# Optimization experiments

Hardware: AMD Instinct MI355X
Metric: run time of the kernel (lower is better)

## Reference

```python
import jax, jax.numpy as jnp
import numpy as np

HID = 2048
NH = 16
NKV = 16
HD = HID // NH          # 128
ROPE_BASE = 100000.0
ROPE_SCALE = 4.0
B, L = 2, 2048
NEG = -1e9


def rope(x, offset=0):
    # x: [B, NH, L, HD]; half-split (rotate-half) RoPE with linear scaling
    Lx = x.shape[2]
    D = HD // 2
    pos = (jnp.arange(offset, offset + Lx, dtype=jnp.float32) / ROPE_SCALE)  # [L]
    freq = jnp.exp(-jnp.arange(D, dtype=jnp.float32) * (np.log(ROPE_BASE) / D))  # [D]
    m_theta = pos[:, None] * freq[None, :]          # [L, D]
    cos, sin = jnp.cos(m_theta), jnp.sin(m_theta)
    x1, x2 = x[..., :D], x[..., D:]
    rx1 = x1 * cos - x2 * sin
    rx2 = x1 * sin + x2 * cos
    return jnp.concatenate([rx1, rx2], axis=-1)


def setup_inputs() -> dict:
    key = jax.random.key(0)
    ks = jax.random.split(key, 5)
    x = jax.random.normal(ks[0], (B, L, HID), dtype=jnp.float32)
    # additive causal mask [1,1,L,L]
    mask = jnp.triu(jnp.full((L, L), NEG, dtype=jnp.float32), k=1)[None, None]
    Wq = jax.random.normal(ks[1], (HID, NH * HD), dtype=jnp.float32) * 0.02
    Wk = jax.random.normal(ks[2], (HID, NKV * HD), dtype=jnp.float32) * 0.02
    Wv = jax.random.normal(ks[3], (HID, NKV * HD), dtype=jnp.float32) * 0.02
    Wo = jax.random.normal(ks[4], (NH * HD, HID), dtype=jnp.float32) * 0.02
    return {"x": x, "mask": mask, "Wq": Wq, "Wk": Wk, "Wv": Wv, "Wo": Wo}


def reference(x, mask, Wq, Wk, Wv, Wo):
    b, l, _ = x.shape
    scale = HD ** -0.5
    q = (x @ Wq).reshape(b, l, NH, HD).transpose(0, 2, 1, 3)    # [B,NH,L,HD]
    k = (x @ Wk).reshape(b, l, NKV, HD).transpose(0, 2, 1, 3)
    v = (x @ Wv).reshape(b, l, NKV, HD).transpose(0, 2, 1, 3)
    rep = NH // NKV
    if rep > 1:
        k = jnp.repeat(k, rep, axis=1)
        v = jnp.repeat(v, rep, axis=1)
    q = rope(q)
    k = rope(k)
    scores = scale * jnp.einsum('bhqd,bhkd->bhqk', q, k)        # [B,NH,L,L]
    scores = scores + mask
    attn = jax.nn.softmax(scores, axis=-1)
    out = jnp.einsum('bhqk,bhkd->bhqd', attn, v)                # [B,NH,L,HD]
    out = out.transpose(0, 2, 1, 3).reshape(b, l, NH * HD)
    return out @ Wo
```

## Files before the change

### kernel.cpp

```cpp
#include <hip/hip_runtime.h>
#include <math.h>

#define BB   2
#define LL   2048
#define HIDD 2048
#define NHH  16
#define HDD  128
#define QKN  4096
#define THR2 11.5416f
#define EST  136

typedef unsigned short u16;
typedef float  f32x4 __attribute__((ext_vector_type(4)));
typedef __bf16 bf16x8 __attribute__((ext_vector_type(8)));

static __device__ __forceinline__ float exp2_fast(float x){
  return __builtin_amdgcn_exp2f(x);
}
static __device__ __forceinline__ u16 f2bf(float x){
  unsigned u = __float_as_uint(x);
  return (u16)((u + 0x7fffu + ((u >> 16) & 1u)) >> 16);
}
static __device__ __forceinline__ float bf2f(u16 b){
  return __uint_as_float(((unsigned)b) << 16);
}
static __device__ __forceinline__ void gl_lds16(const void* g, void* l){
  __builtin_amdgcn_global_load_lds(
      (__attribute__((address_space(1))) void*)(void*)g,
      (__attribute__((address_space(3))) void*)l,
      16, 0, 0);
}


__global__ void cvt_f32_bf16_k(const float* __restrict__ src, u16* __restrict__ dst, int n4){
  int i = blockIdx.x * blockDim.x + threadIdx.x;
  if (i >= n4) return;
  float4 v = ((const float4*)src)[i];
  ushort4 o;
  o.x = f2bf(v.x); o.y = f2bf(v.y); o.z = f2bf(v.z); o.w = f2bf(v.w);
  ((ushort4*)dst)[i] = o;
}

__global__ void rope_table_k(float2* __restrict__ tab){
  int idx = blockIdx.x * blockDim.x + threadIdx.x;
  int l = idx >> 6, d = idx & 63;
  float fr = __expf(-(float)d * 0.17988946f);
  float th = (float)l * 0.25f * fr;
  float s, c;
  sincosf(th, &s, &c);
  tab[idx] = make_float2(c, s);
}

__global__ __launch_bounds__(256) void transpose_cvt4_k(
    const float* __restrict__ Wq, const float* __restrict__ Wk,
    const float* __restrict__ Wv, const float* __restrict__ Wo,
    u16* __restrict__ Wt, u16* __restrict__ Wot)
{
  __shared__ u16 t[64][66];
  const int z = blockIdx.z;
  const float* src = (z == 0) ? Wq : (z == 1) ? Wk : (z == 2) ? Wv : Wo;
  u16* dst = (z == 3) ? Wot : (Wt + (size_t)z * 2048 * 2048);
  const int c0 = blockIdx.x * 64, r0 = blockIdx.y * 64;
  const int tid = threadIdx.x;

  #pragma unroll
  for (int i = 0; i < 4; i++){
    int r  = i * 16 + (tid >> 4);
    int c4 = (tid & 15) * 4;
    float4 v = *(const float4*)&src[(size_t)(r0 + r) * 2048 + c0 + c4];
    t[c4 + 0][r] = f2bf(v.x);
    t[c4 + 1][r] = f2bf(v.y);
    t[c4 + 2][r] = f2bf(v.z);
    t[c4 + 3][r] = f2bf(v.w);
  }
  __syncthreads();
  #pragma unroll
  for (int i = 0; i < 2; i++){
    int c  = i * 32 + (tid >> 3);
    int rs = (tid & 7) * 8;
    const unsigned* p = (const unsigned*)&t[c][rs];
    unsigned w0 = p[0], w1 = p[1], w2 = p[2], w3 = p[3];
    u16* d = &dst[(size_t)(c0 + c) * 2048 + r0 + rs];
    ((unsigned*)d)[0] = w0; ((unsigned*)d)[1] = w1;
    ((unsigned*)d)[2] = w2; ((unsigned*)d)[3] = w3;
  }
}


__global__ __launch_bounds__(256) void gemm_qkv_k(
    const u16* __restrict__ A, const u16* __restrict__ Bt,
    u16* __restrict__ qk, u16* __restrict__ vt,
    const float2* __restrict__ rtab, int M, int N, int K)
{
  __shared__ __align__(16) u16 SH[17408];
  u16* As = SH;
  u16* Bs = SH + 8192;
  const int tid = threadIdx.x, lane = tid & 63, wv = tid >> 6;
  const int wr = wv >> 1, wc = wv & 1;
  const int m0 = blockIdx.y * 128, n0 = blockIdx.x * 128;
  const int rq = lane >> 4, cl = lane & 15;

  const f32x4 Z = {0.f, 0.f, 0.f, 0.f};
  f32x4 acc[4][4];
  #pragma unroll
  for (int m = 0; m < 4; m++)
    #pragma unroll
    for (int n = 0; n < 4; n++) acc[m][n] = Z;

  for (int kt = 0; kt < K; kt += 64){
    #pragma unroll
    for (int i = 0; i < 4; i++){
      int fb = (i * 4 + wv) * 64;
      int p  = (fb + lane) * 16;
      int r  = p >> 7;
      int cbs = (p & 127) ^ ((r & 7) << 4);
      gl_lds16(A  + (size_t)(m0 + r) * K + kt + (cbs >> 1), &As[fb * 8]);
      gl_lds16(Bt + (size_t)(n0 + r) * K + kt + (cbs >> 1), &Bs[fb * 8]);
    }
    __syncthreads();
    #pragma unroll
    for (int ks = 0; ks < 2; ks++){
      const int kb = ks * 64 + rq * 16;
      bf16x8 a[4], b[4];
      #pragma unroll
      for (int m = 0; m < 4; m++){
        int r = wr * 64 + m * 16 + cl;
        a[m] = *(const bf16x8*)((const char*)As + r * 128 + (kb ^ ((r & 7) << 4)));
      }
      #pragma unroll
      for (int n = 0; n < 4; n++){
        int r = wc * 64 + n * 16 + cl;
        b[n] = *(const bf16x8*)((const char*)Bs + r * 128 + (kb ^ ((r & 7) << 4)));
      }
      #pragma unroll
      for (int m = 0; m < 4; m++)
        #pragma unroll
        for (int n = 0; n < 4; n++)
          acc[m][n] = __builtin_amdgcn_mfma_f32_16x16x32_bf16(a[m], b[n], acc[m][n], 0, 0, 0);
    }
    __syncthreads();
  }

  const int hd  = n0 >> 7;
  const int sec = hd >> 4;
  const int hh  = hd & 15;

  #pragma unroll
  for (int m = 0; m < 4; m++){
    int gr0 = wr * 64 + m * 16 + rq * 4;
    #pragma unroll
    for (int n = 0; n < 4; n++){
      int gc = wc * 64 + n * 16 + cl;
      #pragma unroll
      for (int rr = 0; rr < 4; rr++)
        SH[(gr0 + rr) * EST + gc] = f2bf(acc[m][n][rr]);
    }
  }
  __syncthreads();

  if (sec < 2){
    const float fsc = (sec == 0) ? 0.12753375f : 1.0f;
    const int r = tid >> 1, dbase = (tid & 1) * 32;
    const int l = (m0 + r) & (LL - 1);
    const float2* tab = rtab + l * 64 + dbase;
    const u16* srow = &SH[r * EST];
    u16* orow = qk + (size_t)(m0 + r) * QKN + hd * 128;
    #pragma unroll
    for (int g = 0; g < 4; g++){
      bf16x8 x1v = *(const bf16x8*)(srow + dbase + g * 8);
      bf16x8 x2v = *(const bf16x8*)(srow + dbase + 64 + g * 8);
      bf16x8 o1, o2;
      #pragma unroll
      for (int i = 0; i < 8; i++){
        float2 cs = tab[g * 8 + i];
        float x1 = (float)x1v[i], x2 = (float)x2v[i];
        o1[i] = (__bf16)((x1 * cs.x - x2 * cs.y) * fsc);
        o2[i] = (__bf16)((x1 * cs.y + x2 * cs.x) * fsc);
      }
      *(bf16x8*)(orow + dbase + g * 8)      = o1;
      *(bf16x8*)(orow + dbase + 64 + g * 8) = o2;
    }
  } else {
    const int d = tid >> 1, l0 = (tid & 1) * 64;
    const int bh = ((m0 >> 11) << 4) + hh;
    u16* vrow = vt + ((size_t)bh * HDD + d) * LL + (m0 & (LL - 1)) + l0;
    #pragma unroll
    for (int g = 0; g < 8; g++){
      bf16x8 o;
      #pragma unroll
      for (int i = 0; i < 8; i++)
        o[i] = *(__bf16*)&SH[(l0 + g * 8 + i) * EST + d];
      *(bf16x8*)(vrow + g * 8) = o;
    }
  }
}


#define G2_STAGE(kt, bsel) do {                                                           \
  _Pragma("unroll")                                                                       \
  for (int i_ = 0; i_ < 2; i_++){                            \
    int c_ = ((i_ * 8 + wv) * 64) + lane;                                                 \
    int p_ = c_ * 16;                                                                     \
    int r_ = p_ >> 7; int cb_ = (p_ & 127) ^ ((r_ & 7) << 4);                             \
    gl_lds16(A + (size_t)(m0 + r_) * K + (kt) + (cb_ >> 1),                               \
             &AB[bsel][((i_ * 8 + wv) * 64) * 8]);                                        \
  }                                                                                       \
  _Pragma("unroll")                                                                       \
  for (int i_ = 0; i_ < 4; i_++){                            \
    int c_ = ((i_ * 8 + wv) * 64) + lane;                                                 \
    int p_ = c_ * 16;                                                                     \
    int r_ = p_ >> 7; int cb_ = (p_ & 127) ^ ((r_ & 7) << 4);                             \
    gl_lds16(Bt + (size_t)(n0 + r_) * K + (kt) + (cb_ >> 1),                              \
             &AB[bsel][8192 + ((i_ * 8 + wv) * 64) * 8]);                                 \
  }                                                                                       \
} while(0)

template<int OUT_BF16>
__global__ __launch_bounds__(512, 1) void gemm_bt2_k(
    const u16* __restrict__ A, const u16* __restrict__ Bt,
    void* __restrict__ Cout, int M, int N, int K)
{
  __shared__ __align__(16) u16 AB[2][24576];
  const int tid = threadIdx.x, lane = tid & 63, wv = tid >> 6;
  const int wr = wv >> 2, wc = wv & 3;
  const int m0 = blockIdx.y * 128, n0 = blockIdx.x * 256;
  const int rq = lane >> 4, cl = lane & 15;
  const int NT = K >> 6;

  const f32x4 Z = {0.f, 0.f, 0.f, 0.f};
  f32x4 acc[4][4];
  #pragma unroll
  for (int m = 0; m < 4; m++)
    #pragma unroll
    for (int n = 0; n < 4; n++) acc[m][n] = Z;

  G2_STAGE(0, 0);
  G2_STAGE(64, 1);
  asm volatile("s_waitcnt vmcnt(6)");
  __builtin_amdgcn_sched_barrier(0);
  __builtin_amdgcn_s_barrier();

  int cur = 0;
  for (int t = 0; t < NT; t++){
    const char* As_ = (const char*)&AB[cur][0];
    const char* Bs_ = (const char*)&AB[cur][8192];

    #pragma unroll
    for (int ks = 0; ks < 2; ks++){
      const int kb = ks * 64 + rq * 16;
      bf16x8 a[4], b[4];
      #pragma unroll
      for (int m = 0; m < 4; m++){
        int r = wr * 64 + m * 16 + cl;
        a[m] = *(const bf16x8*)(As_ + r * 128 + (kb ^ ((r & 7) << 4)));
      }
      #pragma unroll
      for (int n = 0; n < 4; n++){
        int r = wc * 64 + n * 16 + cl;
        b[n] = *(const bf16x8*)(Bs_ + r * 128 + (kb ^ ((r & 7) << 4)));
      }
      __builtin_amdgcn_s_setprio(1);
      #pragma unroll
      for (int m = 0; m < 4; m++)
        #pragma unroll
        for (int n = 0; n < 4; n++)
          acc[m][n] = __builtin_amdgcn_mfma_f32_16x16x32_bf16(a[m], b[n], acc[m][n], 0, 0, 0);
      __builtin_amdgcn_s_setprio(0);
    }

    __builtin_amdgcn_sched_barrier(0);
    __builtin_amdgcn_s_barrier();

    if (t + 2 < NT){
      G2_STAGE((t + 2) * 64, cur);
      asm volatile("s_waitcnt vmcnt(6)");
    } else {
      asm volatile("s_waitcnt vmcnt(0)");
    }
    __builtin_amdgcn_sched_barrier(0);
    __builtin_amdgcn_s_barrier();
    cur ^= 1;
  }

  #pragma unroll
  for (int m = 0; m < 4; m++){
    int gr0 = m0 + wr * 64 + m * 16 + rq * 4;
    #pragma unroll
    for (int n = 0; n < 4; n++){
      int gc = n0 + wc * 64 + n * 16 + cl;
      #pragma unroll
      for (int rr = 0; rr < 4; rr++){
        if (OUT_BF16) ((u16*)Cout)[(size_t)(gr0 + rr) * N + gc] = f2bf(acc[m][n][rr]);
        else          ((float*)Cout)[(size_t)(gr0 + rr) * N + gc] = acc[m][n][rr];
      }
    }
  }
}


#define STAGE_K(jj, bsel) do {                                                            \
  _Pragma("unroll")                                                                       \
  for (int i_ = 0; i_ < 4; i_++){                                                         \
    int fb_ = (i_ * 4 + wv) * 64;                                                         \
    int p_  = (fb_ + lane) * 16;                                                          \
    int r_ = p_ >> 8; int cb_ = (p_ & 255) ^ ((r_ & 7) << 4);                             \
    gl_lds16(qk + (size_t)(b * LL + (jj) * 64 + r_) * QKN + 2048 + h * HDD + (cb_ >> 1),  \
             &Kb[bsel][fb_ * 8]);                                                         \
  }                                                                                       \
} while(0)

#define STAGE_V(jj, bsel) do {                                                            \
  _Pragma("unroll")                                                                       \
  for (int i_ = 0; i_ < 4; i_++){                                                         \
    int fb_ = (i_ * 4 + wv) * 64;                                                         \
    int p_  = (fb_ + lane) * 16;                                                          \
    int r_ = p_ >> 7; int cb_ = (p_ & 127) ^ ((r_ & 7) << 4);                             \
    gl_lds16(vt + (size_t)(bh * HDD + r_) * LL + (jj) * 64 + (cb_ >> 1),                  \
             &Vb[bsel][fb_ * 8]);                                                         \
  }                                                                                       \
} while(0)

__global__ __launch_bounds__(256, 2) void attn_k(
    const u16* __restrict__ qk, const u16* __restrict__ vt,
    u16* __restrict__ aout)
{
  __shared__ __align__(16) u16 Kb[2][64 * 128];
  __shared__ __align__(16) u16 Vb[2][128 * 64];
  __shared__ __align__(16) u16 Ps[4][1024];
  const int tid = threadIdx.x, lane = tid & 63, wv = tid >> 6;
  const int bh = blockIdx.x;
  const int pr = blockIdx.y;
  const int b = bh >> 4, h = bh & 15;
  const int rq = lane >> 4, cl = lane & 15;

  bf16x8 ones;
  #pragma unroll
  for (int i = 0; i < 8; i++) ones[i] = (__bf16)1.0f;
  const f32x4 Z = {0.f, 0.f, 0.f, 0.f};

  int cur = 0;
  STAGE_V(0, 0);
  STAGE_K(0, 0);

  #pragma unroll
  for (int ph = 0; ph < 2; ph++){
    const int qt = ph ? pr : (31 - pr);
    const int nj = qt + 1;

    bf16x8 qf[4];
    {
      const u16* qb = qk + (size_t)(b * LL + qt * 64 + wv * 16 + cl) * QKN + h * HDD + rq * 8;
      #pragma unroll
      for (int ks = 0; ks < 4; ks++) qf[ks] = *(const bf16x8*)(qb + ks * 32);
    }

    f32x4 acco[8], accl;
    float mst[4];
    #pragma unroll
    for (int n = 0; n < 8; n++) acco[n] = Z;
    accl = Z;
    #pragma unroll
    for (int rr = 0; rr < 4; rr++) mst[rr] = -INFINITY;

    for (int j = 0; j < nj; j++){
      const bool sn = (j + 1 < nj) || (ph == 0);
      if (j + 1 < nj){      STAGE_V(j + 1, cur ^ 1); STAGE_K(j + 1, cur ^ 1); }
      else if (ph == 0){    STAGE_V(0,     cur ^ 1); STAGE_K(0,     cur ^ 1); }
      __builtin_amdgcn_sched_barrier(0);
      if (sn) asm volatile("s_waitcnt vmcnt(8)" ::: "memory");
      else    asm volatile("s_waitcnt vmcnt(0)" ::: "memory");
      __builtin_amdgcn_sched_barrier(0);
      __builtin_amdgcn_s_barrier();
      __builtin_amdgcn_sched_barrier(0);

      f32x4 sv[4];
      {
        const char* KsC = (const char*)&Kb[cur][0];
        #pragma unroll
        for (int ct = 0; ct < 4; ct++) sv[ct] = Z;
        #pragma unroll
        for (int ks = 0; ks < 4; ks++){
          const int kb = ks * 64 + rq * 16;
          #pragma unroll
          for (int ct = 0; ct < 4; ct++){
            int r = ct * 16 + cl;
            bf16x8 bfr = *(const bf16x8*)(KsC + r * 256 + (kb ^ ((r & 7) << 4)));
            sv[ct] = __builtin_amdgcn_mfma_f32_16x16x32_bf16(qf[ks], bfr, sv[ct], 0, 0, 0);
          }
        }
      }

      {
        char* pbase = (char*)&Ps[wv][0];
        const bool msk = (j == qt);

        float p4[4][4], lmx[4];
        #pragma unroll
        for (int rr = 0; rr < 4; rr++) lmx[rr] = -1e30f;
        const int qg = qt * 64 + wv * 16 + rq * 4;
        #pragma unroll
        for (int ct = 0; ct < 4; ct++){
          int col = j * 64 + ct * 16 + cl;
          #pragma unroll
          for (int rr = 0; rr < 4; rr++){
            float v = sv[ct][rr];
            if (msk && col > qg + rr) v = -1e30f;
            p4[ct][rr] = v;
            lmx[rr] = fmaxf(lmx[rr], v);
          }
        }
        float need = -1e30f;
        #pragma unroll
        for (int rr = 0; rr < 4; rr++) need = fmaxf(need, lmx[rr] - mst[rr]);
        if (__any(need > THR2)){
          float mx[4];
          #pragma unroll
          for (int rr = 0; rr < 4; rr++) mx[rr] = lmx[rr];
          #pragma unroll
          for (int off = 1; off < 16; off <<= 1)
            #pragma unroll
            for (int rr = 0; rr < 4; rr++)
              mx[rr] = fmaxf(mx[rr], __shfl_xor(mx[rr], off, 64));
          #pragma unroll
          for (int rr = 0; rr < 4; rr++){
            float mn  = fmaxf(mst[rr], mx[rr]);
            float fsc = exp2_fast(mst[rr] - mn);
            mst[rr] = mn;
            accl[rr] *= fsc;
            #pragma unroll
            for (int n = 0; n < 8; n++) acco[n][rr] *= fsc;
          }
        }
        #pragma unroll
        for (int ct = 0; ct < 4; ct++)
          #pragma unroll
          for (int rr = 0; rr < 4; rr++){
            float e = exp2_fast(p4[ct][rr] - mst[rr]);
            int wr = rq * 4 + rr;
            *(u16*)(pbase + wr * 128 + (((ct * 16 + cl) * 2) ^ ((wr & 7) << 4))) = f2bf(e);
          }
      }

      {
        const char* VsC = (const char*)&Vb[cur][0];
        char* pbase = (char*)&Ps[wv][0];
        #pragma unroll
        for (int ks = 0; ks < 2; ks++){
          const int kvb = ks * 64 + rq * 16;
          bf16x8 pa = *(const bf16x8*)(pbase + cl * 128 + (kvb ^ ((cl & 7) << 4)));
          accl = __builtin_amdgcn_mfma_f32_16x16x32_bf16(pa, ones, accl, 0, 0, 0);
          #pragma unroll
          for (int n = 0; n < 8; n++){
            int r = n * 16 + cl;
            bf16x8 bfr = *(const bf16x8*)(VsC + r * 128 + (kvb ^ ((r & 7) << 4)));
            acco[n] = __builtin_amdgcn_mfma_f32_16x16x32_bf16(pa, bfr, acco[n], 0, 0, 0);
          }
        }
      }

      __builtin_amdgcn_sched_barrier(0);
      __builtin_amdgcn_s_barrier();
      __builtin_amdgcn_sched_barrier(0);
      cur ^= 1;
    }

    #pragma unroll
    for (int rr = 0; rr < 4; rr++){
      float inv = 1.0f / accl[rr];
      size_t grow = (size_t)(b * LL + qt * 64 + wv * 16 + rq * 4 + rr);
      #pragma unroll
      for (int n = 0; n < 8; n++)
        aout[grow * HIDD + h * HDD + n * 16 + cl] = f2bf(acco[n][rr] * inv);
    }
  }
}


extern "C" void kernel_launch(void* const* d_in, const int* in_sizes, int n_in,
                              void* d_out, int out_size, void* d_ws, size_t ws_size,
                              hipStream_t stream)
{
  const float* x  = (const float*)d_in[0];
  const float* Wq = (const float*)d_in[2];
  const float* Wk = (const float*)d_in[3];
  const float* Wv = (const float*)d_in[4];
  const float* Wo = (const float*)d_in[5];
  float* out = (float*)d_out;

  if (ws_size < 120586240ull) return;

  char* ws = (char*)d_ws;
  u16*    xb   = (u16*)(ws);
  u16*    Wt   = (u16*)(ws + 16777216ull);
  u16*    Wot  = (u16*)(ws + 41943040ull);
  u16*    qk   = (u16*)(ws + 50331648ull);
  u16*    vt   = (u16*)(ws + 83886080ull);
  u16*    aout = (u16*)(ws + 100663296ull);
  float2* rtab = (float2*)(ws + 117440512ull);

  cvt_f32_bf16_k<<<2097152 / 256, 256, 0, stream>>>(x, xb, 2097152);
  rope_table_k<<<131072 / 256, 256, 0, stream>>>(rtab);
  transpose_cvt4_k<<<dim3(32, 32, 4), 256, 0, stream>>>(Wq, Wk, Wv, Wo, Wt, Wot);

  gemm_qkv_k<<<dim3(6144 / 128, 4096 / 128), 256, 0, stream>>>(xb, Wt, qk, vt, rtab, 4096, 6144, 2048);

  attn_k<<<dim3(32, 16), 256, 0, stream>>>(qk, vt, aout);

  gemm_bt2_k<0><<<dim3(2048 / 256, 4096 / 128), 512, 0, stream>>>(aout, Wot, out, 4096, 2048, 2048);
}
```

Before: 259.5 us.

## Rewrite QKV GEMM with 256x256 tiles and ping-pong LDS prefetch pipeline

```diff
diff --git a/kernel.cpp b/kernel.cpp
--- a/kernel.cpp
+++ b/kernel.cpp
@@ -8,7 +8,7 @@
 #define HDD  128
 #define QKN  4096
 #define THR2 11.5416f
-#define EST  136
+#define EST2 264
 
 typedef unsigned short u16;
 typedef float  f32x4 __attribute__((ext_vector_type(4)));
@@ -87,110 +87,229 @@
 }
 
 
-__global__ __launch_bounds__(256) void gemm_qkv_k(
+#define STG_HALF(base_u16, src, rowbase, kt_) do {                                        \
+  _Pragma("unroll")                                                                       \
+  for (int i_ = 0; i_ < 2; i_++){                                                         \
+    int cb0_ = i_ * 512 + wv * 64;                           \
+    int c_   = cb0_ + lane;                                                               \
+    int r_   = c_ >> 3;                                       \
+    int cb_  = ((c_ & 7) << 4) ^ ((r_ & 7) << 4);                                         \
+    gl_lds16((src) + (size_t)((rowbase) + r_) * K + (kt_) + (cb_ >> 1),                   \
+             &SH[(base_u16) + cb0_ * 8]);                                                 \
+  }                                                                                       \
+} while(0)
+
+__global__ __launch_bounds__(512, 1) void gemm_qkv256_k(
     const u16* __restrict__ A, const u16* __restrict__ Bt,
     u16* __restrict__ qk, u16* __restrict__ vt,
-    const float2* __restrict__ rtab, int M, int N, int K)
+    const float2* __restrict__ rtab, int K)
 {
-  __shared__ __align__(16) u16 SH[17408];
-  u16* As = SH;
-  u16* Bs = SH + 8192;
+  __shared__ __align__(16) u16 SH[65536];
   const int tid = threadIdx.x, lane = tid & 63, wv = tid >> 6;
-  const int wr = wv >> 1, wc = wv & 1;
-  const int m0 = blockIdx.y * 128, n0 = blockIdx.x * 128;
+  const int wsr = wv >> 2, wsc = wv & 3;
+  const int m0 = blockIdx.y * 256, n0 = blockIdx.x * 256;
   const int rq = lane >> 4, cl = lane & 15;
+  const int NT = K >> 6;
 
   const f32x4 Z = {0.f, 0.f, 0.f, 0.f};
-  f32x4 acc[4][4];
-  #pragma unroll
-  for (int m = 0; m < 4; m++)
-    #pragma unroll
-    for (int n = 0; n < 4; n++) acc[m][n] = Z;
-
-  for (int kt = 0; kt < K; kt += 64){
-    #pragma unroll
-    for (int i = 0; i < 4; i++){
-      int fb = (i * 4 + wv) * 64;
-      int p  = (fb + lane) * 16;
-      int r  = p >> 7;
-      int cbs = (p & 127) ^ ((r & 7) << 4);
-      gl_lds16(A  + (size_t)(m0 + r) * K + kt + (cbs >> 1), &As[fb * 8]);
-      gl_lds16(Bt + (size_t)(n0 + r) * K + kt + (cbs >> 1), &Bs[fb * 8]);
-    }
+  f32x4 acc[2][2][4][2];
+  #pragma unroll
+  for (int i = 0; i < 2; i++)
+    #pragma unroll
+    for (int j = 0; j < 2; j++)
+      #pragma unroll
+      for (int mf = 0; mf < 4; mf++)
+        #pragma unroll
+        for (int nf = 0; nf < 2; nf++) acc[i][j][mf][nf] = Z;
+
+  STG_HALF(0,                 A,  m0 + 0,   0);
+  STG_HALF(32768,             Bt, n0 + 0,   0);
+  STG_HALF(8192,              A,  m0 + 128, 0);
+  STG_HALF(32768 + 8192,      Bt, n0 + 128, 0);
+  STG_HALF(16384,             A,  m0 + 0,   64);
+  STG_HALF(32768 + 16384,     Bt, n0 + 0,   64);
+
+  for (int t = 0; t < NT; t++){
+    const int X = t & 1;
+    const char* Ab = (const char*)SH + X * 32768;
+    const char* Bb = (const char*)SH + 65536 + X * 32768;
+    bf16x8 af[4][2], bfb[2][2];
+
+    __builtin_amdgcn_sched_barrier(0);
+    if (t == NT - 1) asm volatile("s_waitcnt vmcnt(0)" ::: "memory");
+    else             asm volatile("s_waitcnt vmcnt(4)" ::: "memory");
+    __builtin_amdgcn_sched_barrier(0);
+    __builtin_amdgcn_s_barrier();
+    __builtin_amdgcn_sched_barrier(0);
+    #pragma unroll
+    for (int mf = 0; mf < 4; mf++){
+      int gr = wsr * 64 + mf * 16 + cl;
+      #pragma unroll
+      for (int ks = 0; ks < 2; ks++)
+        af[mf][ks] = *(const bf16x8*)(Ab + gr * 128 + ((ks * 64 + rq * 16) ^ ((gr & 7) << 4)));
+    }
+    #pragma unroll
+    for (int nf = 0; nf < 2; nf++){
+      int gc = wsc * 32 + nf * 16 + cl;
+      #pragma unroll
+      for (int ks = 0; ks < 2; ks++)
+        bfb[nf][ks] = *(const bf16x8*)(Bb + gc * 128 + ((ks * 64 + rq * 16) ^ ((gc & 7) << 4)));
+    }
+    if (t + 1 < NT) STG_HALF(((t + 1) & 1) * 16384 + 8192, A, m0 + 128, (t + 1) * 64);
+    __builtin_amdgcn_sched_barrier(0);
+    asm volatile("s_waitcnt lgkmcnt(0)" ::: "memory");
+    __builtin_amdgcn_sched_barrier(0);
+    __builtin_amdgcn_s_setprio(1);
+    #pragma unroll
+    for (int mf = 0; mf < 4; mf++)
+      #pragma unroll
+      for (int nf = 0; nf < 2; nf++)
+        #pragma unroll
+        for (int ks = 0; ks < 2; ks++)
+          acc[0][0][mf][nf] = __builtin_amdgcn_mfma_f32_16x16x32_bf16(af[mf][ks], bfb[nf][ks], acc[0][0][mf][nf], 0, 0, 0);
+    __builtin_amdgcn_s_setprio(0);
+    __builtin_amdgcn_sched_barrier(0);
+
+    __builtin_amdgcn_s_barrier();
+    __builtin_amdgcn_sched_barrier(0);
+    #pragma unroll
+    for (int nf = 0; nf < 2; nf++){
+      int gc = 128 + wsc * 32 + nf * 16 + cl;
+      #pragma unroll
+      for (int ks = 0; ks < 2; ks++)
+        bfb[nf][ks] = *(const bf16x8*)(Bb + gc * 128 + ((ks * 64 + rq * 16) ^ ((gc & 7) << 4)));
+    }
+    if (t + 1 < NT) STG_HALF(32768 + ((t + 1) & 1) * 16384 + 8192, Bt, n0 + 128, (t + 1) * 64);
+    __builtin_amdgcn_sched_barrier(0);
+    asm volatile("s_waitcnt lgkmcnt(0)" ::: "memory");
+    __builtin_amdgcn_sched_barrier(0);
+    __builtin_amdgcn_s_setprio(1);
+    #pragma unroll
+    for (int mf = 0; mf < 4; mf++)
+      #pragma unroll
+      for (int nf = 0; nf < 2; nf++)
+        #pragma unroll
+        for (int ks = 0; ks < 2; ks++)
+          acc[0][1][mf][nf] = __builtin_amdgcn_mfma_f32_16x16x32_bf16(af[mf][ks], bfb[nf][ks], acc[0][1][mf][nf], 0, 0, 0);
+    __builtin_amdgcn_s_setprio(0);
+    __builtin_amdgcn_sched_barrier(0);
+
+    __builtin_amdgcn_s_barrier();
+    __builtin_amdgcn_sched_barrier(0);
+    #pragma unroll
+    for (int mf = 0; mf < 4; mf++){
+      int gr = 128 + wsr * 64 + mf * 16 + cl;
+      #pragma unroll
+      for (int ks = 0; ks < 2; ks++)
+        af[mf][ks] = *(const bf16x8*)(Ab + gr * 128 + ((ks * 64 + rq * 16) ^ ((gr & 7) << 4)));
+    }
+    #pragma unroll
+    for (int nf = 0; nf < 2; nf++){
+      int gc = wsc * 32 + nf * 16 + cl;
+      #pragma unroll
+      for (int ks = 0; ks < 2; ks++)
+        bfb[nf][ks] = *(const bf16x8*)(Bb + gc * 128 + ((ks * 64 + rq * 16) ^ ((gc & 7) << 4)));
+    }
+    if (t + 2 < NT) STG_HALF((t & 1) * 16384, A, m0 + 0, (t + 2) * 64);
+    __builtin_amdgcn_sched_barrier(0);
+    asm volatile("s_waitcnt lgkmcnt(0)" ::: "memory");
+    __builtin_amdgcn_sched_barrier(0);
+    __builtin_amdgcn_s_setprio(1);
+    #pragma unroll
+    for (int mf = 0; mf < 4; mf++)
+      #pragma unroll
+      for (int nf = 0; nf < 2; nf++)
+        #pragma unroll
+        for (int ks = 0; ks < 2; ks++)
+          acc[1][0][mf][nf] = __builtin_amdgcn_mfma_f32_16x16x32_bf16(af[mf][ks], bfb[nf][ks], acc[1][0][mf][nf], 0, 0, 0);
+    __builtin_amdgcn_s_setprio(0);
+    __builtin_amdgcn_sched_barrier(0);
+
+    __builtin_amdgcn_s_barrier();
+    __builtin_amdgcn_sched_barrier(0);
+    #pragma unroll
+    for (int nf = 0; nf < 2; nf++){
+      int gc = 128 + wsc * 32 + nf * 16 + cl;
+      #pragma unroll
+      for (int ks = 0; ks < 2; ks++)
+        bfb[nf][ks] = *(const bf16x8*)(Bb + gc * 128 + ((ks * 64 + rq * 16) ^ ((gc & 7) << 4)));
+    }
+    if (t + 2 < NT) STG_HALF(32768 + (t & 1) * 16384, Bt, n0 + 0, (t + 2) * 64);
+    __builtin_amdgcn_sched_barrier(0);
+    asm volatile("s_waitcnt lgkmcnt(0)" ::: "memory");
+    __builtin_amdgcn_sched_barrier(0);
+    __builtin_amdgcn_s_setprio(1);
+    #pragma unroll
+    for (int mf = 0; mf < 4; mf++)
+      #pragma unroll
+      for (int nf = 0; nf < 2; nf++)
+        #pragma unroll
+        for (int ks = 0; ks < 2; ks++)
+          acc[1][1][mf][nf] = __builtin_amdgcn_mfma_f32_16x16x32_bf16(af[mf][ks], bfb[nf][ks], acc[1][1][mf][nf], 0, 0, 0);
+    __builtin_amdgcn_s_setprio(0);
+    __builtin_amdgcn_sched_barrier(0);
+  }
+
+  const int sec = n0 >> 11;
+  const int hd2 = n0 >> 7;
+  u16* ES = SH;
+
+  #pragma unroll
+  for (int ih = 0; ih < 2; ih++){
     __syncthreads();
     #pragma unroll
-    for (int ks = 0; ks < 2; ks++){
-      const int kb = ks * 64 + rq * 16;
-      bf16x8 a[4], b[4];
-      #pragma unroll
-      for (int m = 0; m < 4; m++){
-        int r = wr * 64 + m * 16 + cl;
-        a[m] = *(const bf16x8*)((const char*)As + r * 128 + (kb ^ ((r & 7) << 4)));
-      }
-      #pragma unroll
-      for (int n = 0; n < 4; n++){
-        int r = wc * 64 + n * 16 + cl;
-        b[n] = *(const bf16x8*)((const char*)Bs + r * 128 + (kb ^ ((r & 7) << 4)));
-      }
-      #pragma unroll
-      for (int m = 0; m < 4; m++)
-        #pragma unroll
-        for (int n = 0; n < 4; n++)
-          acc[m][n] = __builtin_amdgcn_mfma_f32_16x16x32_bf16(a[m], b[n], acc[m][n], 0, 0, 0);
-    }
+    for (int j = 0; j < 2; j++)
+      #pragma unroll
+      for (int mf = 0; mf < 4; mf++){
+        int er = wsr * 64 + mf * 16 + rq * 4;
+        #pragma unroll
+        for (int nf = 0; nf < 2; nf++){
+          int ec = j * 128 + wsc * 32 + nf * 16 + cl;
+          #pragma unroll
+          for (int rr = 0; rr < 4; rr++)
+            ES[(er + rr) * EST2 + ec] = f2bf(acc[ih][j][mf][nf][rr]);
+        }
+      }
     __syncthreads();
-  }
-
-  const int hd  = n0 >> 7;
-  const int sec = hd >> 4;
-  const int hh  = hd & 15;
-
-  #pragma unroll
-  for (int m = 0; m < 4; m++){
-    int gr0 = wr * 64 + m * 16 + rq * 4;
-    #pragma unroll
-    for (int n = 0; n < 4; n++){
-      int gc = wc * 64 + n * 16 + cl;
-      #pragma unroll
-      for (int rr = 0; rr < 4; rr++)
-        SH[(gr0 + rr) * EST + gc] = f2bf(acc[m][n][rr]);
-    }
-  }
-  __syncthreads();
-
-  if (sec < 2){
-    const float fsc = (sec == 0) ? 0.12753375f : 1.0f;
-    const int r = tid >> 1, dbase = (tid & 1) * 32;
-    const int l = (m0 + r) & (LL - 1);
-    const float2* tab = rtab + l * 64 + dbase;
-    const u16* srow = &SH[r * EST];
-    u16* orow = qk + (size_t)(m0 + r) * QKN + hd * 128;
-    #pragma unroll
-    for (int g = 0; g < 4; g++){
-      bf16x8 x1v = *(const bf16x8*)(srow + dbase + g * 8);
-      bf16x8 x2v = *(const bf16x8*)(srow + dbase + 64 + g * 8);
-      bf16x8 o1, o2;
-      #pragma unroll
-      for (int i = 0; i < 8; i++){
-        float2 cs = tab[g * 8 + i];
-        float x1 = (float)x1v[i], x2 = (float)x2v[i];
-        o1[i] = (__bf16)((x1 * cs.x - x2 * cs.y) * fsc);
-        o2[i] = (__bf16)((x1 * cs.y + x2 * cs.x) * fsc);
-      }
-      *(bf16x8*)(orow + dbase + g * 8)      = o1;
-      *(bf16x8*)(orow + dbase + 64 + g * 8) = o2;
-    }
-  } else {
-    const int d = tid >> 1, l0 = (tid & 1) * 64;
-    const int bh = ((m0 >> 11) << 4) + hh;
-    u16* vrow = vt + ((size_t)bh * HDD + d) * LL + (m0 & (LL - 1)) + l0;
-    #pragma unroll
-    for (int g = 0; g < 8; g++){
-      bf16x8 o;
-      #pragma unroll
-      for (int i = 0; i < 8; i++)
-        o[i] = *(__bf16*)&SH[(l0 + g * 8 + i) * EST + d];
-      *(bf16x8*)(vrow + g * 8) = o;
+
+    if (sec < 2){
+      const float fsc = (sec == 0) ? 0.12753375f : 1.0f;
+      const int r = tid >> 2, cq = tid & 3;
+      const int j = cq >> 1, dbase = (cq & 1) * 32;
+      const int grow = m0 + ih * 128 + r;
+      const int l = grow & (LL - 1);
+      const float2* tab = rtab + l * 64 + dbase;
+      const u16* srow = &ES[r * EST2 + j * 128];
+      u16* orow = qk + (size_t)grow * QKN + n0 + j * 128;
+      #pragma unroll
+      for (int g = 0; g < 4; g++){
+        bf16x8 x1v = *(const bf16x8*)(srow + dbase + g * 8);
+        bf16x8 x2v = *(const bf16x8*)(srow + dbase + 64 + g * 8);
+        bf16x8 o1, o2;
+        #pragma unroll
+        for (int i8 = 0; i8 < 8; i8++){
+          float2 cs = tab[g * 8 + i8];
+          float x1 = (float)x1v[i8], x2 = (float)x2v[i8];
+          o1[i8] = (__bf16)((x1 * cs.x - x2 * cs.y) * fsc);
+          o2[i8] = (__bf16)((x1 * cs.y + x2 * cs.x) * fsc);
+        }
+        *(bf16x8*)(orow + dbase + g * 8)      = o1;
+        *(bf16x8*)(orow + dbase + 64 + g * 8) = o2;
+      }
+    } else {
+      const int c = tid >> 1, lh = tid & 1;
+      const int j = c >> 7, d = c & 127;
+      const int grow0 = m0 + ih * 128;
+      const int bh = ((grow0 >> 11) << 4) + (hd2 - 32 + j);
+      u16* vrow = vt + ((size_t)bh * HDD + d) * LL + (grow0 & (LL - 1)) + lh * 64;
+      #pragma unroll
+      for (int g = 0; g < 8; g++){
+        bf16x8 o;
+        #pragma unroll
+        for (int i8 = 0; i8 < 8; i8++)
+          o[i8] = *(__bf16*)&ES[(lh * 64 + g * 8 + i8) * EST2 + c];
+        *(bf16x8*)(vrow + g * 8) = o;
+      }
     }
   }
 }
@@ -502,7 +621,7 @@
   rope_table_k<<<131072 / 256, 256, 0, stream>>>(rtab);
   transpose_cvt4_k<<<dim3(32, 32, 4), 256, 0, stream>>>(Wq, Wk, Wv, Wo, Wt, Wot);
 
-  gemm_qkv_k<<<dim3(6144 / 128, 4096 / 128), 256, 0, stream>>>(xb, Wt, qk, vt, rtab, 4096, 6144, 2048);
+  gemm_qkv256_k<<<dim3(6144 / 256, 4096 / 256), 512, 0, stream>>>(xb, Wt, qk, vt, rtab, 2048);
 
   attn_k<<<dim3(32, 16), 256, 0, stream>>>(qk, vt, aout);
 
```

Measured after the change: 256.3 us (median of 3 runs). No clear change (-1.2%).

## Permute B rows so RoPE pairs land in registers, skip LDS staging for Q/K

Applied to the files above, without the earlier changes.

```diff
diff --git a/kernel.cpp b/kernel.cpp
--- a/kernel.cpp
+++ b/kernel.cpp
@@ -114,8 +114,9 @@
       int p  = (fb + lane) * 16;
       int r  = p >> 7;
       int cbs = (p & 127) ^ ((r & 7) << 4);
+      int sg = ((r >> 6) << 5) + (((r >> 4) & 1) << 4) + (((r >> 5) & 1) << 6) + (r & 15);
       gl_lds16(A  + (size_t)(m0 + r) * K + kt + (cbs >> 1), &As[fb * 8]);
-      gl_lds16(Bt + (size_t)(n0 + r) * K + kt + (cbs >> 1), &Bs[fb * 8]);
+      gl_lds16(Bt + (size_t)(n0 + sg) * K + kt + (cbs >> 1), &Bs[fb * 8]);
     }
     __syncthreads();
     #pragma unroll
@@ -145,42 +146,39 @@
   const int sec = hd >> 4;
   const int hh  = hd & 15;
 
-  #pragma unroll
-  for (int m = 0; m < 4; m++){
-    int gr0 = wr * 64 + m * 16 + rq * 4;
-    #pragma unroll
-    for (int n = 0; n < 4; n++){
-      int gc = wc * 64 + n * 16 + cl;
-      #pragma unroll
-      for (int rr = 0; rr < 4; rr++)
-        SH[(gr0 + rr) * EST + gc] = f2bf(acc[m][n][rr]);
-    }
-  }
-  __syncthreads();
-
   if (sec < 2){
     const float fsc = (sec == 0) ? 0.12753375f : 1.0f;
-    const int r = tid >> 1, dbase = (tid & 1) * 32;
-    const int l = (m0 + r) & (LL - 1);
-    const float2* tab = rtab + l * 64 + dbase;
-    const u16* srow = &SH[r * EST];
-    u16* orow = qk + (size_t)(m0 + r) * QKN + hd * 128;
-    #pragma unroll
-    for (int g = 0; g < 4; g++){
-      bf16x8 x1v = *(const bf16x8*)(srow + dbase + g * 8);
-      bf16x8 x2v = *(const bf16x8*)(srow + dbase + 64 + g * 8);
-      bf16x8 o1, o2;
-      #pragma unroll
-      for (int i = 0; i < 8; i++){
-        float2 cs = tab[g * 8 + i];
-        float x1 = (float)x1v[i], x2 = (float)x2v[i];
-        o1[i] = (__bf16)((x1 * cs.x - x2 * cs.y) * fsc);
-        o2[i] = (__bf16)((x1 * cs.y + x2 * cs.x) * fsc);
-      }
-      *(bf16x8*)(orow + dbase + g * 8)      = o1;
-      *(bf16x8*)(orow + dbase + 64 + g * 8) = o2;
+    const int d0 = wc * 32 + cl;
+    #pragma unroll
+    for (int m = 0; m < 4; m++){
+      #pragma unroll
+      for (int rr = 0; rr < 4; rr++){
+        int row = wr * 64 + m * 16 + rq * 4 + rr;
+        int l = (m0 + row) & (LL - 1);
+        float2 cs0 = rtab[l * 64 + d0];
+        float2 cs1 = rtab[l * 64 + d0 + 16];
+        float x1a = acc[m][0][rr], x2a = acc[m][2][rr];
+        float x1b = acc[m][1][rr], x2b = acc[m][3][rr];
+        u16* orow = qk + (size_t)(m0 + row) * QKN + hd * 128;
+        orow[d0]      = f2bf((x1a * cs0.x - x2a * cs0.y) * fsc);
+        orow[d0 + 64] = f2bf((x1a * cs0.y + x2a * cs0.x) * fsc);
+        orow[d0 + 16] = f2bf((x1b * cs1.x - x2b * cs1.y) * fsc);
+        orow[d0 + 80] = f2bf((x1b * cs1.y + x2b * cs1.x) * fsc);
+      }
     }
   } else {
+    #pragma unroll
+    for (int m = 0; m < 4; m++){
+      int gr0 = wr * 64 + m * 16 + rq * 4;
+      #pragma unroll
+      for (int n = 0; n < 4; n++){
+        int ec = wc * 32 + (n & 1) * 16 + (n >> 1) * 64 + cl;
+        #pragma unroll
+        for (int rr = 0; rr < 4; rr++)
+          SH[(gr0 + rr) * EST + ec] = f2bf(acc[m][n][rr]);
+      }
+    }
+    __syncthreads();
     const int d = tid >> 1, l0 = (tid & 1) * 64;
     const int bh = ((m0 >> 11) << 4) + hh;
     u16* vrow = vt + ((size_t)bh * HDD + d) * LL + (m0 & (LL - 1)) + l0;
```

Measured after the change: 256.6 us. Within noise of the previous version (-1.1%).
